# Kernel optimization log

Measured on AMD Instinct MI355X. Metric: run time of the kernel, lower is better.

Reference implementation:

```python
import jax, jax.numpy as jnp
import numpy as np

B, S, D_MODEL = 2, 1024, 3072
HEADS, HEAD_DIM = 24, 128
EPS = 1e-6


def _rms_norm(x, w):
    # RMSNorm over last dim (head_dim), elementwise affine
    var = jnp.mean(jnp.square(x), axis=-1, keepdims=True)
    return x * jax.lax.rsqrt(var + EPS) * w


def _apply_rotary(x, freqs_cis):
    # x: [B, S, H, D]; freqs_cis: [S, 1, rot_dim] broadcasting over B via leading dims
    rot_dim = freqs_cis.shape[-1]
    xr, x_pass = x[..., :rot_dim], x[..., rot_dim:]
    cos_ = jnp.cos(freqs_cis).astype(x.dtype)
    sin_ = jnp.sin(freqs_cis).astype(x.dtype)
    x1, x2 = jnp.split(xr, 2, axis=-1)
    x_rot = jnp.concatenate((-x2, x1), axis=-1)
    return jnp.concatenate((xr * cos_ + x_rot * sin_, x_pass), axis=-1)


def setup_inputs() -> dict:
    key = jax.random.key(0)
    ks = jax.random.split(key, 8)
    inner = HEADS * HEAD_DIM
    scale = 1.0 / np.sqrt(D_MODEL)
    return {
        "hidden_states": jax.random.normal(ks[0], (B, S, D_MODEL), dtype=jnp.float32),
        "image_rotary_emb": jax.random.uniform(ks[1], (S, 1, HEAD_DIM), dtype=jnp.float32) * 6.283,
        "Wq": jax.random.normal(ks[2], (inner, D_MODEL), dtype=jnp.float32) * scale,
        "Wk": jax.random.normal(ks[3], (inner, D_MODEL), dtype=jnp.float32) * scale,
        "Wv": jax.random.normal(ks[4], (inner, D_MODEL), dtype=jnp.float32) * scale,
        "Wo": jax.random.normal(ks[5], (D_MODEL, inner), dtype=jnp.float32) * scale,
        "norm_q_w": jnp.ones((HEAD_DIM,), dtype=jnp.float32),
        "norm_k_w": jnp.ones((HEAD_DIM,), dtype=jnp.float32),
    }


def reference(hidden_states, image_rotary_emb, Wq, Wk, Wv, Wo, norm_q_w, norm_k_w):
    # QKV projections: [B,S,Dm] @ [Dm,inner] -> [B,S,H,Dh]
    q = jnp.einsum("bsd,ed->bse", hidden_states, Wq).reshape(B, S, HEADS, HEAD_DIM)
    k = jnp.einsum("bsd,ed->bse", hidden_states, Wk).reshape(B, S, HEADS, HEAD_DIM)
    v = jnp.einsum("bsd,ed->bse", hidden_states, Wv).reshape(B, S, HEADS, HEAD_DIM)
    # per-head RMSNorm on q/k
    q = _rms_norm(q, norm_q_w)
    k = _rms_norm(k, norm_k_w)
    # RoPE (Megatron rotate_half, full head dim rotated)
    q = _apply_rotary(q, image_rotary_emb)
    k = _apply_rotary(k, image_rotary_emb)
    # SDPA (non-causal, no mask): [B,H,S,S]
    scale = 1.0 / np.sqrt(HEAD_DIM)
    scores = jnp.einsum("bqhd,bkhd->bhqk", q, k) * scale
    attn = jax.nn.softmax(scores, axis=-1)
    out = jnp.einsum("bhqk,bkhd->bqhd", attn, v).reshape(B, S, HEADS * HEAD_DIM)
    return jnp.einsum("bse,de->bsd", out, Wo)
```

## Files before the change

### kernel.cpp

```cpp
#include <hip/hip_runtime.h>
#include <hip/hip_bf16.h>
#include <math.h>

#define B_   2
#define S_   1024
#define DM_  3072
#define H_   24
#define HD_  128
#define BH_  (B_*H_)
#define MROWS (B_*S_)
#define QSCALE 0.08838834764831845f

typedef __attribute__((ext_vector_type(8))) short short8;
typedef __attribute__((ext_vector_type(4))) float f32x4;

__device__ __forceinline__ unsigned short f2bf(float f) {
    union { float f; unsigned u; } v; v.f = f;
    unsigned r = v.u + 0x7fffu + ((v.u >> 16) & 1u);
    return (unsigned short)(r >> 16);
}

#define GLD_LDS16(gptr, ldsptr)                                                            \
    __builtin_amdgcn_global_load_lds(                                                      \
        (const __attribute__((address_space(1))) unsigned int*)(gptr),                     \
        (__attribute__((address_space(3))) unsigned int*)(ldsptr), 16, 0, 0)

__global__ __launch_bounds__(256) void cvt_bf16(const float* __restrict__ src,
                                                unsigned short* __restrict__ dst, int n4) {
    int i = blockIdx.x * 256 + threadIdx.x;
    if (i >= n4) return;
    float4 v = ((const float4*)src)[i];
    ushort4 o;
    o.x = f2bf(v.x); o.y = f2bf(v.y); o.z = f2bf(v.z); o.w = f2bf(v.w);
    ((ushort4*)dst)[i] = o;
}

__global__ __launch_bounds__(256) void rope_tab(const float* __restrict__ freqs,
                                                float2* __restrict__ tab) {
    int i = blockIdx.x * 256 + threadIdx.x;
    float f = freqs[i];
    tab[i] = make_float2(cosf(f), sinf(f));
}

__global__ __launch_bounds__(256) void gemm_bt(const unsigned short* __restrict__ A,
                                               const unsigned short* __restrict__ Bm,
                                               float* __restrict__ C,
                                               int Ndim, int K) {
    __shared__ __align__(16) unsigned short As[128 * 64];
    __shared__ __align__(16) unsigned short Bs[128 * 64];
    const int t = threadIdx.x;
    const int m0 = blockIdx.y * 128, n0 = blockIdx.x * 128;
    const int w = t >> 6, lane = t & 63, quad = lane >> 4, ln = lane & 15;
    const int wm = (w >> 1) * 64, wn = (w & 1) * 64;
    const int rl = lane >> 3;
    const int gc = (lane & 7) ^ rl;
    const int cs = ln & 7;

    f32x4 acc[4][4];
#pragma unroll
    for (int i = 0; i < 4; ++i)
#pragma unroll
        for (int j = 0; j < 4; ++j) acc[i][j] = (f32x4){0.f, 0.f, 0.f, 0.f};

    const unsigned short* ga = &A[(long long)(m0 + w * 32 + rl) * K + gc * 8];
    const unsigned short* gb = &Bm[(long long)(n0 + w * 32 + rl) * K + gc * 8];

    const int nkt = K >> 6;
    for (int kt = 0; kt < nkt; ++kt) {
#pragma unroll
        for (int c = 0; c < 4; ++c) {
            const int r0 = w * 32 + c * 8;
            GLD_LDS16(ga + (long long)(c * 8) * K, &As[r0 * 64]);
            GLD_LDS16(gb + (long long)(c * 8) * K, &Bs[r0 * 64]);
        }
        ga += 64; gb += 64;
        __syncthreads();
#pragma unroll
        for (int ks = 0; ks < 2; ++ks) {
            short8 a[4], b[4];
#pragma unroll
            for (int i = 0; i < 4; ++i) {
                int row = wm + i * 16 + ln;
                a[i] = *(const short8*)&As[row * 64 + (((ks * 4 + quad) ^ cs) << 3)];
            }
#pragma unroll
            for (int j = 0; j < 4; ++j) {
                int row = wn + j * 16 + ln;
                b[j] = *(const short8*)&Bs[row * 64 + (((ks * 4 + quad) ^ cs) << 3)];
            }
#pragma unroll
            for (int i = 0; i < 4; ++i)
#pragma unroll
                for (int j = 0; j < 4; ++j)
                    acc[i][j] = __builtin_amdgcn_mfma_f32_16x16x32_bf16(a[i], b[j], acc[i][j], 0, 0, 0);
        }
        __syncthreads();
    }
#pragma unroll
    for (int i = 0; i < 4; ++i) {
#pragma unroll
        for (int reg = 0; reg < 4; ++reg) {
            int row = m0 + wm + i * 16 + quad * 4 + reg;
            float* crow = C + (long long)row * Ndim + n0 + wn + ln;
#pragma unroll
            for (int j = 0; j < 4; ++j) crow[j * 16] = acc[i][j][reg];
        }
    }
}

__global__ __launch_bounds__(256) void norm_rope(const float* __restrict__ qkvf,
                                                 const float2* __restrict__ tab,
                                                 const float* __restrict__ wqv,
                                                 const float* __restrict__ wkv,
                                                 unsigned short* __restrict__ Qb,
                                                 unsigned short* __restrict__ Kb,
                                                 unsigned short* __restrict__ Vtb) {
    const int w = threadIdx.x >> 6, t = threadIdx.x & 63;
    const int row = blockIdx.x * 4 + w;
    const int h = row % H_;
    const int bs = row / H_;
    const int s = bs % S_;
    const int b = bs / S_;
    const float* qrow = qkvf + (long long)bs * (3 * DM_) + h * HD_;
    float2 cs1 = tab[s * HD_ + t];
    float2 cs2 = tab[s * HD_ + t + 64];
    const long long qo = ((long long)(b * H_ + h) * S_ + s) * HD_;
    {
        float x1 = qrow[t], x2 = qrow[t + 64];
        float ss = x1 * x1 + x2 * x2;
#pragma unroll
        for (int off = 32; off; off >>= 1) ss += __shfl_xor(ss, off);
        float rr = rsqrtf(ss * (1.f / 128.f) + 1e-6f);
        float y1 = x1 * rr * wqv[t], y2 = x2 * rr * wqv[t + 64];
        Qb[qo + t]      = f2bf((y1 * cs1.x - y2 * cs1.y) * QSCALE);
        Qb[qo + t + 64] = f2bf((y2 * cs2.x + y1 * cs2.y) * QSCALE);
    }
    {
        const float* krow = qrow + DM_;
        float x1 = krow[t], x2 = krow[t + 64];
        float ss = x1 * x1 + x2 * x2;
#pragma unroll
        for (int off = 32; off; off >>= 1) ss += __shfl_xor(ss, off);
        float rr = rsqrtf(ss * (1.f / 128.f) + 1e-6f);
        float y1 = x1 * rr * wkv[t], y2 = x2 * rr * wkv[t + 64];
        Kb[qo + t]      = f2bf(y1 * cs1.x - y2 * cs1.y);
        Kb[qo + t + 64] = f2bf(y2 * cs2.x + y1 * cs2.y);
    }
    {
        const float* vrow = qrow + 2 * DM_;
        long long vo = (long long)(b * H_ + h) * HD_;
        Vtb[(vo + t) * S_ + s]      = f2bf(vrow[t]);
        Vtb[(vo + t + 64) * S_ + s] = f2bf(vrow[t + 64]);
    }
}

__global__ __launch_bounds__(256) void attn(const unsigned short* __restrict__ Qb,
                                            const unsigned short* __restrict__ Kb,
                                            const unsigned short* __restrict__ Vtb,
                                            unsigned short* __restrict__ Ob) {
    __shared__ __align__(16) unsigned short Ks[64][136];
    __shared__ __align__(16) unsigned short Vts[128][72];
    __shared__ __align__(16) unsigned short Ps[4][16][72];
    const int bh = blockIdx.x, qt = blockIdx.y;
    const int t = threadIdx.x, w = t >> 6, lane = t & 63, quad = lane >> 4, ln = lane & 15;
    const int b = bh / H_, h = bh - b * H_;

    short8 qfrag[4];
    const long long qbase = ((long long)bh * S_ + qt * 64 + w * 16 + ln) * HD_;
#pragma unroll
    for (int ks = 0; ks < 4; ++ks)
        qfrag[ks] = *(const short8*)&Qb[qbase + ks * 32 + quad * 8];

    f32x4 o[8];
#pragma unroll
    for (int n = 0; n < 8; ++n) o[n] = (f32x4){0.f, 0.f, 0.f, 0.f};
    float m_run[4], l_run[4];
#pragma unroll
    for (int r = 0; r < 4; ++r) { m_run[r] = -1e30f; l_run[r] = 0.f; }

    for (int kt = 0; kt < S_ / 64; ++kt) {
        __syncthreads();
#pragma unroll
        for (int c = 0; c < 4; ++c) {
            int i = c * 256 + t;
            int r = i >> 4, cg = (i & 15) << 3;
            *(uint4*)&Ks[r][cg] = *(const uint4*)&Kb[((long long)bh * S_ + kt * 64 + r) * HD_ + cg];
            int r2 = i >> 3, cg2 = (i & 7) << 3;
            *(uint4*)&Vts[r2][cg2] = *(const uint4*)&Vtb[((long long)bh * HD_ + r2) * S_ + kt * 64 + cg2];
        }
        __syncthreads();
        f32x4 sj[4];
#pragma unroll
        for (int j = 0; j < 4; ++j) {
            f32x4 sa = (f32x4){0.f, 0.f, 0.f, 0.f};
#pragma unroll
            for (int ks = 0; ks < 4; ++ks) {
                short8 bb = *(const short8*)&Ks[j * 16 + ln][ks * 32 + quad * 8];
                sa = __builtin_amdgcn_mfma_f32_16x16x32_bf16(qfrag[ks], bb, sa, 0, 0, 0);
            }
            sj[j] = sa;
        }
        float al[4];
#pragma unroll
        for (int r = 0; r < 4; ++r) {
            float m = fmaxf(fmaxf(sj[0][r], sj[1][r]), fmaxf(sj[2][r], sj[3][r]));
#pragma unroll
            for (int off = 8; off; off >>= 1) m = fmaxf(m, __shfl_xor(m, off, 16));
            float mn = fmaxf(m_run[r], m);
            al[r] = __expf(m_run[r] - mn);
            m_run[r] = mn;
            float sum = 0.f;
#pragma unroll
            for (int j = 0; j < 4; ++j) {
                float p = __expf(sj[j][r] - mn);
                sj[j][r] = p;
                sum += p;
            }
#pragma unroll
            for (int off = 8; off; off >>= 1) sum += __shfl_xor(sum, off, 16);
            l_run[r] = l_run[r] * al[r] + sum;
        }
#pragma unroll
        for (int n = 0; n < 8; ++n)
#pragma unroll
            for (int r = 0; r < 4; ++r) o[n][r] *= al[r];
#pragma unroll
        for (int j = 0; j < 4; ++j)
#pragma unroll
            for (int r = 0; r < 4; ++r)
                Ps[w][quad * 4 + r][j * 16 + ln] = f2bf(sj[j][r]);
        __asm__ volatile("s_waitcnt lgkmcnt(0)" ::: "memory");
#pragma unroll
        for (int ks = 0; ks < 2; ++ks) {
            short8 pf = *(const short8*)&Ps[w][ln][ks * 32 + quad * 8];
#pragma unroll
            for (int n = 0; n < 8; ++n) {
                short8 vf = *(const short8*)&Vts[n * 16 + ln][ks * 32 + quad * 8];
                o[n] = __builtin_amdgcn_mfma_f32_16x16x32_bf16(pf, vf, o[n], 0, 0, 0);
            }
        }
    }
    float inv[4];
#pragma unroll
    for (int r = 0; r < 4; ++r) inv[r] = 1.f / l_run[r];
    const int row_s = qt * 64 + w * 16 + quad * 4;
#pragma unroll
    for (int n = 0; n < 8; ++n)
#pragma unroll
        for (int r = 0; r < 4; ++r) {
            long long off = ((long long)b * S_ + row_s + r) * DM_ + h * HD_ + n * 16 + ln;
            Ob[off] = f2bf(o[n][r] * inv[r]);
        }
}

extern "C" void kernel_launch(void* const* d_in, const int* in_sizes, int n_in,
                              void* d_out, int out_size, void* d_ws, size_t ws_size,
                              hipStream_t stream) {
    const float* hs    = (const float*)d_in[0];
    const float* freqs = (const float*)d_in[1];
    const float* Wq    = (const float*)d_in[2];
    const float* Wk    = (const float*)d_in[3];
    const float* Wv    = (const float*)d_in[4];
    const float* Wo    = (const float*)d_in[5];
    const float* nqw   = (const float*)d_in[6];
    const float* nkw   = (const float*)d_in[7];
    float* out = (float*)d_out;

    char* ws = (char*)d_ws;
    unsigned short* Xb    = (unsigned short*)(ws);
    unsigned short* Wqkvb = (unsigned short*)(ws + 12582912LL);
    unsigned short* Wob   = (unsigned short*)(ws + 69206016LL);
    float*          qkvf  = (float*)        (ws + 88080384LL);
    unsigned short* Qb    = (unsigned short*)(ws + 163577856LL);
    unsigned short* Kb    = (unsigned short*)(ws + 176160768LL);
    unsigned short* Vtb   = (unsigned short*)(ws + 188743680LL);
    unsigned short* Ob    = (unsigned short*)(ws + 201326592LL);
    float2*         rtab  = (float2*)        (ws + 213909504LL);

    cvt_bf16<<<6144, 256, 0, stream>>>(hs, Xb, 1572864);
    cvt_bf16<<<9216, 256, 0, stream>>>(Wq, Wqkvb,            2359296);
    cvt_bf16<<<9216, 256, 0, stream>>>(Wk, Wqkvb +  9437184, 2359296);
    cvt_bf16<<<9216, 256, 0, stream>>>(Wv, Wqkvb + 18874368, 2359296);
    cvt_bf16<<<9216, 256, 0, stream>>>(Wo, Wob,              2359296);
    rope_tab<<<512, 256, 0, stream>>>(freqs, rtab);
    gemm_bt<<<dim3(72, 16), 256, 0, stream>>>(Xb, Wqkvb, qkvf, 3 * DM_, DM_);
    norm_rope<<<(B_ * S_ * H_) / 4, 256, 0, stream>>>(qkvf, rtab, nqw, nkw, Qb, Kb, Vtb);
    attn<<<dim3(BH_, S_ / 64), 256, 0, stream>>>(Qb, Kb, Vtb, Ob);
    gemm_bt<<<dim3(24, 16), 256, 0, stream>>>(Ob, Wob, out, DM_, DM_);
}
```

Before: 559.0 us.

## Fuse per-head RMSNorm, RoPE and V transpose into QKV GEMM epilogue

The QKV GEMM epilogue now computes the per-head RMSNorm, applies RoPE and writes bf16 Q/K directly, and writes V transposed. This removes the fp32 qkv intermediate and the separate norm_rope kernel. The B tile rows are permuted so each wave pair holds columns d and d+64 for the rotate-half pairing, with a cross-wave sum of squares through shared memory. The cost is scattered bf16 stores in the epilogue, including strided V transpose writes.

```diff
diff --git a/kernel.cpp b/kernel.cpp
--- a/kernel.cpp
+++ b/kernel.cpp
@@ -8,7 +8,7 @@
 #define H_   24
 #define HD_  128
 #define BH_  (B_*H_)
-#define MROWS (B_*S_)
+#define KDIM 3072
 #define QSCALE 0.08838834764831845f
 
 typedef __attribute__((ext_vector_type(8))) short short8;
@@ -42,19 +42,30 @@
     tab[i] = make_float2(cosf(f), sinf(f));
 }
 
-__global__ __launch_bounds__(256) void gemm_bt(const unsigned short* __restrict__ A,
-                                               const unsigned short* __restrict__ Bm,
-                                               float* __restrict__ C,
-                                               int Ndim, int K) {
+template <int FUSED>
+__global__ __launch_bounds__(256) void gemm_fused(const unsigned short* __restrict__ A,
+                                                  const unsigned short* __restrict__ Bm,
+                                                  float* __restrict__ C, int Ndim,
+                                                  const float2* __restrict__ rtab,
+                                                  const float* __restrict__ nqw,
+                                                  const float* __restrict__ nkw,
+                                                  unsigned short* __restrict__ Qb,
+                                                  unsigned short* __restrict__ Kb,
+                                                  unsigned short* __restrict__ Vtb) {
     __shared__ __align__(16) unsigned short As[128 * 64];
     __shared__ __align__(16) unsigned short Bs[128 * 64];
+    __shared__ float pse[4][64];
     const int t = threadIdx.x;
-    const int m0 = blockIdx.y * 128, n0 = blockIdx.x * 128;
+    const int bx = blockIdx.x;
+    const int m0 = blockIdx.y * 128, n0 = bx * 128;
     const int w = t >> 6, lane = t & 63, quad = lane >> 4, ln = lane & 15;
-    const int wm = (w >> 1) * 64, wn = (w & 1) * 64;
+    const int wm = (w >> 1) * 64;
+    const int p = w & 1;
+    const int dj0 = p ? 32 : 0;
     const int rl = lane >> 3;
     const int gc = (lane & 7) ^ rl;
     const int cs = ln & 7;
+    const int woff = (w == 1) ? 32 : (w == 2) ? -32 : 0;
 
     f32x4 acc[4][4];
 #pragma unroll
@@ -62,16 +73,15 @@
 #pragma unroll
         for (int j = 0; j < 4; ++j) acc[i][j] = (f32x4){0.f, 0.f, 0.f, 0.f};
 
-    const unsigned short* ga = &A[(long long)(m0 + w * 32 + rl) * K + gc * 8];
-    const unsigned short* gb = &Bm[(long long)(n0 + w * 32 + rl) * K + gc * 8];
-
-    const int nkt = K >> 6;
-    for (int kt = 0; kt < nkt; ++kt) {
+    const unsigned short* ga = &A[(long long)(m0 + w * 32 + rl) * KDIM + gc * 8];
+    const unsigned short* gb = &Bm[(long long)(n0 + w * 32 + woff + rl) * KDIM + gc * 8];
+
+    for (int kt = 0; kt < KDIM / 64; ++kt) {
 #pragma unroll
         for (int c = 0; c < 4; ++c) {
             const int r0 = w * 32 + c * 8;
-            GLD_LDS16(ga + (long long)(c * 8) * K, &As[r0 * 64]);
-            GLD_LDS16(gb + (long long)(c * 8) * K, &Bs[r0 * 64]);
+            GLD_LDS16(ga + (long long)(c * 8) * KDIM, &As[r0 * 64]);
+            GLD_LDS16(gb + (long long)(c * 8) * KDIM, &Bs[r0 * 64]);
         }
         ga += 64; gb += 64;
         __syncthreads();
@@ -85,7 +95,7 @@
             }
 #pragma unroll
             for (int j = 0; j < 4; ++j) {
-                int row = wn + j * 16 + ln;
+                int row = p * 64 + j * 16 + ln;
                 b[j] = *(const short8*)&Bs[row * 64 + (((ks * 4 + quad) ^ cs) << 3)];
             }
 #pragma unroll
@@ -96,61 +106,82 @@
         }
         __syncthreads();
     }
-#pragma unroll
-    for (int i = 0; i < 4; ++i) {
-#pragma unroll
-        for (int reg = 0; reg < 4; ++reg) {
-            int row = m0 + wm + i * 16 + quad * 4 + reg;
-            float* crow = C + (long long)row * Ndim + n0 + wn + ln;
-#pragma unroll
-            for (int j = 0; j < 4; ++j) crow[j * 16] = acc[i][j][reg];
-        }
+
+    if (!FUSED) {
+#pragma unroll
+        for (int i = 0; i < 4; ++i)
+#pragma unroll
+            for (int reg = 0; reg < 4; ++reg) {
+                int row = m0 + wm + i * 16 + quad * 4 + reg;
+                float* crow = C + (long long)row * Ndim + n0 + ln;
+                crow[dj0]      = acc[i][0][reg];
+                crow[dj0 + 16] = acc[i][1][reg];
+                crow[dj0 + 64] = acc[i][2][reg];
+                crow[dj0 + 80] = acc[i][3][reg];
+            }
+        return;
     }
-}
-
-__global__ __launch_bounds__(256) void norm_rope(const float* __restrict__ qkvf,
-                                                 const float2* __restrict__ tab,
-                                                 const float* __restrict__ wqv,
-                                                 const float* __restrict__ wkv,
-                                                 unsigned short* __restrict__ Qb,
-                                                 unsigned short* __restrict__ Kb,
-                                                 unsigned short* __restrict__ Vtb) {
-    const int w = threadIdx.x >> 6, t = threadIdx.x & 63;
-    const int row = blockIdx.x * 4 + w;
-    const int h = row % H_;
-    const int bs = row / H_;
-    const int s = bs % S_;
-    const int b = bs / S_;
-    const float* qrow = qkvf + (long long)bs * (3 * DM_) + h * HD_;
-    float2 cs1 = tab[s * HD_ + t];
-    float2 cs2 = tab[s * HD_ + t + 64];
-    const long long qo = ((long long)(b * H_ + h) * S_ + s) * HD_;
-    {
-        float x1 = qrow[t], x2 = qrow[t + 64];
-        float ss = x1 * x1 + x2 * x2;
-#pragma unroll
-        for (int off = 32; off; off >>= 1) ss += __shfl_xor(ss, off);
-        float rr = rsqrtf(ss * (1.f / 128.f) + 1e-6f);
-        float y1 = x1 * rr * wqv[t], y2 = x2 * rr * wqv[t + 64];
-        Qb[qo + t]      = f2bf((y1 * cs1.x - y2 * cs1.y) * QSCALE);
-        Qb[qo + t + 64] = f2bf((y2 * cs2.x + y1 * cs2.y) * QSCALE);
-    }
-    {
-        const float* krow = qrow + DM_;
-        float x1 = krow[t], x2 = krow[t + 64];
-        float ss = x1 * x1 + x2 * x2;
-#pragma unroll
-        for (int off = 32; off; off >>= 1) ss += __shfl_xor(ss, off);
-        float rr = rsqrtf(ss * (1.f / 128.f) + 1e-6f);
-        float y1 = x1 * rr * wkv[t], y2 = x2 * rr * wkv[t + 64];
-        Kb[qo + t]      = f2bf(y1 * cs1.x - y2 * cs1.y);
-        Kb[qo + t + 64] = f2bf(y2 * cs2.x + y1 * cs2.y);
-    }
-    {
-        const float* vrow = qrow + 2 * DM_;
-        long long vo = (long long)(b * H_ + h) * HD_;
-        Vtb[(vo + t) * S_ + s]      = f2bf(vrow[t]);
-        Vtb[(vo + t + 64) * S_ + s] = f2bf(vrow[t + 64]);
+    const int region = bx / 24;
+    const int h = bx % 24;
+    if (region < 2) {
+#pragma unroll
+        for (int i = 0; i < 4; ++i)
+#pragma unroll
+            for (int reg = 0; reg < 4; ++reg) {
+                float s = 0.f;
+#pragma unroll
+                for (int j = 0; j < 4; ++j) { float v = acc[i][j][reg]; s += v * v; }
+#pragma unroll
+                for (int off = 8; off; off >>= 1) s += __shfl_xor(s, off, 16);
+                if (ln == 0) pse[w][i * 16 + quad * 4 + reg] = s;
+            }
+        __syncthreads();
+        const float* nw = region ? nkw : nqw;
+        unsigned short* outp = region ? Kb : Qb;
+        const float scl = region ? 1.f : QSCALE;
+        const float nw0  = nw[dj0 + ln],      nw1  = nw[dj0 + 16 + ln];
+        const float nw64 = nw[dj0 + 64 + ln], nw80 = nw[dj0 + 80 + ln];
+#pragma unroll
+        for (int i = 0; i < 4; ++i)
+#pragma unroll
+            for (int reg = 0; reg < 4; ++reg) {
+                const int idx = i * 16 + quad * 4 + reg;
+                const float tot = pse[w][idx] + pse[w ^ 1][idx];
+                const float rr = rsqrtf(tot * (1.f / 128.f) + 1e-6f);
+                const int row = m0 + wm + idx;
+                const int b = row >> 10, s = row & 1023;
+                const long long ob = ((long long)(b * H_ + h) * S_ + s) * HD_;
+                {
+                    const int d1 = dj0 + ln;
+                    float y1 = acc[i][0][reg] * rr * nw0;
+                    float y2 = acc[i][2][reg] * rr * nw64;
+                    float2 c1 = rtab[s * HD_ + d1], c2 = rtab[s * HD_ + d1 + 64];
+                    outp[ob + d1]      = f2bf((y1 * c1.x - y2 * c1.y) * scl);
+                    outp[ob + d1 + 64] = f2bf((y2 * c2.x + y1 * c2.y) * scl);
+                }
+                {
+                    const int d1 = dj0 + 16 + ln;
+                    float y1 = acc[i][1][reg] * rr * nw1;
+                    float y2 = acc[i][3][reg] * rr * nw80;
+                    float2 c1 = rtab[s * HD_ + d1], c2 = rtab[s * HD_ + d1 + 64];
+                    outp[ob + d1]      = f2bf((y1 * c1.x - y2 * c1.y) * scl);
+                    outp[ob + d1 + 64] = f2bf((y2 * c2.x + y1 * c2.y) * scl);
+                }
+            }
+    } else {
+#pragma unroll
+        for (int i = 0; i < 4; ++i)
+#pragma unroll
+            for (int reg = 0; reg < 4; ++reg) {
+                const int row = m0 + wm + i * 16 + quad * 4 + reg;
+                const int b = row >> 10, s = row & 1023;
+                const long long vb = (long long)(b * H_ + h) * HD_;
+#pragma unroll
+                for (int j = 0; j < 4; ++j) {
+                    const int d = dj0 + (j & 1) * 16 + (j >> 1) * 64 + ln;
+                    Vtb[(vb + d) * S_ + s] = f2bf(acc[i][j][reg]);
+                }
+            }
     }
 }
 
@@ -262,20 +293,21 @@
     const float* Wk    = (const float*)d_in[3];
     const float* Wv    = (const float*)d_in[4];
     const float* Wo    = (const float*)d_in[5];
+    const float* Wo_   = (const float*)d_in[5];
     const float* nqw   = (const float*)d_in[6];
     const float* nkw   = (const float*)d_in[7];
     float* out = (float*)d_out;
+    (void)Wo_;
 
     char* ws = (char*)d_ws;
     unsigned short* Xb    = (unsigned short*)(ws);
     unsigned short* Wqkvb = (unsigned short*)(ws + 12582912LL);
     unsigned short* Wob   = (unsigned short*)(ws + 69206016LL);
-    float*          qkvf  = (float*)        (ws + 88080384LL);
-    unsigned short* Qb    = (unsigned short*)(ws + 163577856LL);
-    unsigned short* Kb    = (unsigned short*)(ws + 176160768LL);
-    unsigned short* Vtb   = (unsigned short*)(ws + 188743680LL);
-    unsigned short* Ob    = (unsigned short*)(ws + 201326592LL);
-    float2*         rtab  = (float2*)        (ws + 213909504LL);
+    unsigned short* Qb    = (unsigned short*)(ws + 88080384LL);
+    unsigned short* Kb    = (unsigned short*)(ws + 100663296LL);
+    unsigned short* Vtb   = (unsigned short*)(ws + 113246208LL);
+    unsigned short* Ob    = (unsigned short*)(ws + 125829120LL);
+    float2*         rtab  = (float2*)        (ws + 138412032LL);
 
     cvt_bf16<<<6144, 256, 0, stream>>>(hs, Xb, 1572864);
     cvt_bf16<<<9216, 256, 0, stream>>>(Wq, Wqkvb,            2359296);
@@ -283,8 +315,10 @@
     cvt_bf16<<<9216, 256, 0, stream>>>(Wv, Wqkvb + 18874368, 2359296);
     cvt_bf16<<<9216, 256, 0, stream>>>(Wo, Wob,              2359296);
     rope_tab<<<512, 256, 0, stream>>>(freqs, rtab);
-    gemm_bt<<<dim3(72, 16), 256, 0, stream>>>(Xb, Wqkvb, qkvf, 3 * DM_, DM_);
-    norm_rope<<<(B_ * S_ * H_) / 4, 256, 0, stream>>>(qkvf, rtab, nqw, nkw, Qb, Kb, Vtb);
+    gemm_fused<1><<<dim3(72, 16), 256, 0, stream>>>(Xb, Wqkvb, nullptr, 0,
+                                                    rtab, nqw, nkw, Qb, Kb, Vtb);
     attn<<<dim3(BH_, S_ / 64), 256, 0, stream>>>(Qb, Kb, Vtb, Ob);
-    gemm_bt<<<dim3(24, 16), 256, 0, stream>>>(Ob, Wob, out, DM_, DM_);
-}
+    gemm_fused<0><<<dim3(24, 16), 256, 0, stream>>>(Ob, Wob, out, DM_,
+                                                    nullptr, nullptr, nullptr,
+                                                    nullptr, nullptr, nullptr);
+}
```

Result: faster. 508.5 us (-9.0%).
